# Kernel optimization log

Measured on AMD Instinct MI355X. Metric: run time of the kernel, lower is better.

## Reference

```python
import jax, jax.numpy as jnp
import numpy as np

GAMMA = 0.1      # rbf kernel gamma (args.sigma)
REG = 0.1        # diagonal regularizer (args.reg)
C = 1.0          # box constraint (args.C)
ETA = 0.001      # PGD step size (args.eta)
NUM_ITER = 100   # max solver iterations (args.num_iter)
STOP = 0.01      # relative-change stopping condition (args.stop_condition)
BS, D = 384, 256


def setup_inputs() -> dict:
    key = jax.random.key(0)
    k1, k2, k3 = jax.random.split(key, 3)
    return {
        "xis": jax.random.normal(k1, (BS, D), jnp.float32),
        "xjs": jax.random.normal(k2, (BS, D), jnp.float32),
        "alpha_init": jax.random.normal(k3, (BS, BS - 1, 1), jnp.float32),
    }


def _l2norm(x):
    return x / jnp.linalg.norm(x, axis=1, keepdims=True)


def _offdiag_idx(bs):
    # idx[i] = [0..bs-1] with i removed, shape (bs, bs-1); static, built with numpy
    idx = np.stack([np.concatenate([np.arange(i), np.arange(i + 1, bs)]) for i in range(bs)])
    return jnp.asarray(idx, dtype=jnp.int32)


def _pgd_nesterov(DD, lbd, alpha0):
    # min_a 0.5 a^T DD a - lbd^T a  s.t. 0 <= a <= C, batched over anchors,
    # Nesterov momentum beta_t = t/(t+3), early stop on relative change.
    def cond(state):
        t, a, a_prev, rel = state
        return (t < NUM_ITER) & (rel >= STOP)

    def body(state):
        t, a, a_prev, rel = state
        beta = t.astype(jnp.float32) / (t.astype(jnp.float32) + 3.0)
        z = a + beta * (a - a_prev)
        grad = jnp.einsum('bij,bjk->bik', DD, z) - lbd  # (bs, bs-1, 1)
        a_new = jnp.clip(jax.nn.relu(z - ETA * grad), 0.0, C)
        rel = jnp.linalg.norm(a_new - a) / (jnp.linalg.norm(a) + 1e-8)
        return (t + 1, a_new, a, rel)

    state = (jnp.array(0, jnp.int32), alpha0, alpha0, jnp.array(jnp.inf, jnp.float32))
    _, a, _, _ = jax.lax.while_loop(cond, body, state)
    return a


def _forward(xis, xjs, alpha_init):
    zis = _l2norm(xis)
    zjs = _l2norm(xjs)
    bs = zis.shape[0]
    Z = jnp.concatenate([zis, zjs], axis=0)          # (2bs, d)
    # rbf kernel: exp(-gamma * ||x - y||^2)
    sq = (jnp.sum(zis * zis, 1)[:, None] + jnp.sum(Z * Z, 1)[None, :]
          - 2.0 * zis @ Z.T)
    K = jnp.exp(-GAMMA * jnp.maximum(sq, 0.0))        # (bs, 2bs)

    KK = K[:, :bs]                                    # k(zis_i, zis_j)
    KK_d0 = KK * (1.0 - jnp.eye(bs, dtype=K.dtype))   # zero diagonal
    oneone = jnp.ones((bs, bs), K.dtype) + REG * jnp.eye(bs, dtype=K.dtype)
    # Delta[i,j,k] = 1 + reg*d_jk + KK[j,k] - KK_d0[i,j] - KK_d0[i,k]
    Delta = (oneone + KK)[None, :, :] - KK_d0[:, :, None] - KK_d0[:, None, :]

    idx = _offdiag_idx(bs)                            # (bs, bs-1)
    DD = jnp.take_along_axis(Delta, idx[:, :, None], axis=1)
    DD = jnp.take_along_axis(DD, idx[:, None, :], axis=2)  # (bs, bs-1, bs-1)

    alpha0 = jnp.clip(jax.nn.relu(alpha_init), 0.0, C)
    lbd = 2.0 * jnp.ones((bs, bs - 1, 1), K.dtype)
    alpha_y = _pgd_nesterov(jax.lax.stop_gradient(DD), lbd,
                            jax.lax.stop_gradient(alpha0))
    alpha_y = jax.lax.stop_gradient(jnp.clip(jax.nn.relu(alpha_y[:, :, 0]), 0.0, C))
    alpha_x = alpha_y.sum(1)                          # (bs,)

    Ks = K[:, bs:]                                    # k(zis_i, zjs_j), (bs, bs)
    pos_loss = jnp.mean(alpha_x * jnp.diagonal(Ks))
    # Kn[k,i] = Ks[idx[i,k], i]  -> gather off-diagonal of Ks.T per row
    KsT_offdiag = jnp.take_along_axis(Ks.T, idx, axis=1)  # (bs, bs-1)
    neg_loss = jnp.sum(alpha_y * KsT_offdiag) / bs
    return jnp.exp(neg_loss - pos_loss)


def reference(xis, xjs, alpha_init):
    return _forward(xis, xjs, alpha_init)
```

## Files before the change

### kernel.cpp

```cpp
#include <hip/hip_runtime.h>
#include <hip/hip_fp16.h>
#include <math.h>

#define BSZ   384
#define BM1   383
#define DIM   256
#define NZTOT 768
#define NBLK  96
#define RPB   4
#define TPB   768
#define NITER 100
#define RINGD 8
#define ARRFULL NBLK
#define KLDSU (16 * 5 * 384)
#define KRESB (KLDSU * 4)
#define WSHB  (4 * 384 * 4)
#define DYNB  (KRESB + WSHB)

#define OFF_Z    0
#define OFF_NRM  196608
#define OFF_K    197376
#define OFF_KH   492288
#define OFF_A    639744
#define OFF_NUM  786816
#define OFF_DEN  786944
#define OFF_ARR  787072
#define OFF_LOSS 787200

typedef _Float16 half8_t __attribute__((ext_vector_type(8)));
typedef float    f32x4_t __attribute__((ext_vector_type(4)));
__device__ __forceinline__ half8_t u4h8(uint4 v) {
    union { uint4 u; half8_t h; } x; x.u = v; return x.h;
}

__global__ void init_kernel(float* num, float* den, int* arr, double* lossAcc) {
    int t = threadIdx.x;
    if (t < NITER) { num[t] = 0.f; den[t] = 0.f; arr[t] = 0; }
    if (t < 2) lossAcc[t] = 0.0;
}

__global__ void __launch_bounds__(64)
norm_kernel(const float* __restrict__ xis, const float* __restrict__ xjs,
            float* __restrict__ Z, float* __restrict__ nrm2) {
    const int row  = blockIdx.x;
    const int lane = threadIdx.x;
    const float* src = (row < BSZ) ? (xis + (size_t)row * DIM)
                                   : (xjs + (size_t)(row - BSZ) * DIM);
    float4 x = reinterpret_cast<const float4*>(src)[lane];
    float s = x.x*x.x + x.y*x.y + x.z*x.z + x.w*x.w;
    for (int m = 32; m; m >>= 1) s += __shfl_xor(s, m, 64);
    float nrm = sqrtf(s);
    float4 z;
    z.x = x.x / nrm; z.y = x.y / nrm; z.z = x.z / nrm; z.w = x.w / nrm;
    reinterpret_cast<float4*>(Z + (size_t)row * DIM)[lane] = z;
    float s2 = z.x*z.x + z.y*z.y + z.z*z.z + z.w*z.w;
    for (int m = 32; m; m >>= 1) s2 += __shfl_xor(s2, m, 64);
    if (lane == 0) nrm2[row] = s2;
}

__global__ void __launch_bounds__(256)
k_kernel(const float* __restrict__ Z, const float* __restrict__ nrm2,
         float* __restrict__ Km, __half* __restrict__ KP2) {
    const int i = blockIdx.x;
    const int j = blockIdx.y * 256 + threadIdx.x;
    __shared__ float zi[DIM];
    zi[threadIdx.x] = Z[(size_t)i * DIM + threadIdx.x];
    __syncthreads();
    const float4* zr = reinterpret_cast<const float4*>(Z + (size_t)j * DIM);
    float acc = 0.f;
    #pragma unroll 8
    for (int k = 0; k < DIM/4; ++k) {
        float4 v = zr[k];
        acc = fmaf(zi[4*k+0], v.x, acc);
        acc = fmaf(zi[4*k+1], v.y, acc);
        acc = fmaf(zi[4*k+2], v.z, acc);
        acc = fmaf(zi[4*k+3], v.w, acc);
    }
    float sq = nrm2[i] + nrm2[j] - 2.f * acc;
    sq = fmaxf(sq, 0.f);
    const float val = expf(-0.1f * sq);
    Km[(size_t)i * NZTOT + j] = val;
    if (j < BSZ) KP2[(size_t)(i >> 1) * 768 + j * 2 + (i & 1)] = __float2half(val);
}

#define LDSFRAG(dst, s, t) do {                                               \
    const unsigned* _b = kresu + (16*(s) + kgrp*4)*384 + (c0 + 16*(t) + mloc);\
    dst.x = _b[0]; dst.y = _b[384]; dst.z = _b[768]; dst.w = _b[1152];        \
} while (0)

#define GFRAG(dst, s, t) do {                                                 \
    const unsigned* _b = kp2u + (size_t)(16*(s) + kgrp*4)*384 + (c0 + 16*(t) + mloc); \
    dst.x = _b[0]; dst.y = _b[384]; dst.z = _b[768]; dst.w = _b[1152];        \
} while (0)

#define BFRAG(dst, s) do {                                                    \
    dst = *reinterpret_cast<const uint4*>(&zh[rB][16*(s) + kgrp*4]);          \
} while (0)

#define STEP_LDS(s) do { uint4 _bf, _a0, _a1;                                 \
    BFRAG(_bf, s); LDSFRAG(_a0, s, 0); LDSFRAG(_a1, s, 1);                    \
    acc0 = __builtin_amdgcn_mfma_f32_16x16x32_f16(u4h8(_a0), u4h8(_bf), acc0, 0, 0, 0); \
    acc1 = __builtin_amdgcn_mfma_f32_16x16x32_f16(u4h8(_a1), u4h8(_bf), acc1, 0, 0, 0); \
} while (0)

#define STEP_REG(s, QA, QB) do { uint4 _bf;                                   \
    BFRAG(_bf, s);                                                            \
    acc0 = __builtin_amdgcn_mfma_f32_16x16x32_f16(u4h8(QA), u4h8(_bf), acc0, 0, 0, 0); \
    acc1 = __builtin_amdgcn_mfma_f32_16x16x32_f16(u4h8(QB), u4h8(_bf), acc1, 0, 0, 0); \
} while (0)

__global__ void __launch_bounds__(TPB, 1)
pgd_kernel(const float* __restrict__ Km, const __half* __restrict__ KP2,
           const float* __restrict__ alpha_init,
           float* __restrict__ afin, float* num, float* den, int* arr) {
    const int g    = blockIdx.x;
    const int c    = threadIdx.x;
    const int lane = c & 63;
    const int wv   = c >> 6;
    const int mloc = lane & 15;
    const int kgrp = lane >> 4;
    const int c0   = 32 * wv;
    const int rB   = mloc & 3;

    extern __shared__ char dynlc[];
    unsigned* const kresu = (unsigned*)dynlc;
    float* const    wshf  = (float*)(dynlc + KRESB);

    __shared__ unsigned zh[RPB][200];
    __shared__ float  rscr[12][10];
    __shared__ float  SD[8];
    __shared__ unsigned long long scanm[2];

    const bool act = (c < BSZ);
    const unsigned* const kp2u = (const unsigned*)KP2;

    float a[RPB], kb[RPB]; bool vld[RPB];
    #pragma unroll
    for (int r = 0; r < RPB; ++r) {
        const int b = g * RPB + r;
        vld[r] = act && (c != b);
        kb[r]  = act ? Km[(size_t)b * NZTOT + c] : 0.f;
        float v = 0.f;
        if (vld[r]) {
            const int i = c - (c > b ? 1 : 0);
            v = alpha_init[(size_t)b * BM1 + i];
            v = fminf(fmaxf(v, 0.f), 1.f);
        }
        a[r] = v;
    }
    float z[RPB];
    #pragma unroll
    for (int r = 0; r < RPB; ++r) z[r] = a[r];

    unsigned histx[RINGD], histy[RINGD];
    {
        const __half2 h01 = __floats2half2_rn(a[0], a[1]);
        const __half2 h23 = __floats2half2_rn(a[2], a[3]);
        const unsigned px = *reinterpret_cast<const unsigned*>(&h01);
        const unsigned py = *reinterpret_cast<const unsigned*>(&h23);
        #pragma unroll
        for (int s = 0; s < RINGD; ++s) { histx[s] = px; histy[s] = py; }
    }

    {
        const uint4* s4 = reinterpret_cast<const uint4*>(KP2);
        uint4* d4 = reinterpret_cast<uint4*>(kresu);
        #pragma unroll
        for (int i = 0; i < 10; ++i) d4[c + 768 * i] = s4[c + 768 * i];
    }
    uint4 q50,q51, q60,q61, q70,q71, q80,q81;
    GFRAG(q50, 5, 0); GFRAG(q51, 5, 1);
    GFRAG(q60, 6, 0); GFRAG(q61, 6, 1);
    GFRAG(q70, 7, 0); GFRAG(q71, 7, 1);
    GFRAG(q80, 8, 0); GFRAG(q81, 8, 1);

    {
        float an2 = 0.f;
        float vv[10];
        #pragma unroll
        for (int r = 0; r < RPB; ++r) {
            if (act) reinterpret_cast<__half*>(&zh[r][0])[c] = __float2half(z[r]);
            vv[r]     = z[r];
            vv[4 + r] = kb[r] * z[r];
            an2 += a[r] * a[r];
        }
        vv[8] = 0.f; vv[9] = an2;
        #pragma unroll
        for (int k = 0; k < 10; ++k) {
            float x = vv[k];
            x += __shfl_down(x, 32, 64); x += __shfl_down(x, 16, 64);
            x += __shfl_down(x,  8, 64); x += __shfl_down(x,  4, 64);
            x += __shfl_down(x,  2, 64); x += __shfl_down(x,  1, 64);
            if (lane == 0) rscr[wv][k] = x;
        }
        if (c < 2) scanm[c] = 0ULL;
    }
    __syncthreads();

    int stopT = -1;
    int sstate = 0, okv = 0, aval = 0;
    float nnv = 0.f, ddv = 1.f;

    for (int t = 0; t < NITER; ++t) {
        {
            const unsigned long long m0 = scanm[0], m1 = scanm[1];
            const int st = m0 ? (__ffsll(m0) - 1) : (m1 ? 63 + __ffsll(m1) : -1);
            if (st >= 0) { stopT = st; break; }
        }
        if (c < 8) {
            float s = 0.f;
            #pragma unroll
            for (int w = 0; w < 12; ++w) s += rscr[w][c];
            SD[c] = s;
        }
        if (c == 0) {
            float nb = 0.f, db = 0.f;
            #pragma unroll
            for (int w = 0; w < 12; ++w) { nb += rscr[w][8]; db += rscr[w][9]; }
            __hip_atomic_fetch_add(&den[t], db, __ATOMIC_RELAXED, __HIP_MEMORY_SCOPE_AGENT);
            if (t > 0) {
                __hip_atomic_fetch_add(&num[t - 1], nb, __ATOMIC_RELAXED, __HIP_MEMORY_SCOPE_AGENT);
                __hip_atomic_fetch_add(&arr[t - 1], 1, __ATOMIC_RELEASE, __HIP_MEMORY_SCOPE_AGENT);
            }
        }
        if (c < NITER) {
            if (sstate == 0) {
                aval = __hip_atomic_load(&arr[c], __ATOMIC_RELAXED, __HIP_MEMORY_SCOPE_AGENT);
            } else if (sstate == 1) {
                nnv = __hip_atomic_load(&num[c], __ATOMIC_RELAXED, __HIP_MEMORY_SCOPE_AGENT);
                ddv = __hip_atomic_load(&den[c], __ATOMIC_RELAXED, __HIP_MEMORY_SCOPE_AGENT);
            }
        }

        f32x4_t acc0 = {0.f, 0.f, 0.f, 0.f};
        f32x4_t acc1 = {0.f, 0.f, 0.f, 0.f};
        {
            uint4 g90,g91, gA0,gA1, gB0,gB1;
            GFRAG(g90,  9, 0); GFRAG(g91,  9, 1);
            GFRAG(gA0, 10, 0); GFRAG(gA1, 10, 1);
            GFRAG(gB0, 11, 0); GFRAG(gB1, 11, 1);
            STEP_LDS(0); STEP_LDS(1); STEP_LDS(2); STEP_LDS(3); STEP_LDS(4);
            STEP_REG(5, q50, q51);
            STEP_REG(6, q60, q61);
            STEP_REG(7, q70, q71);
            STEP_REG(8, q80, q81);
            STEP_REG(9,  g90, g91);
            STEP_REG(10, gA0, gA1);
            STEP_REG(11, gB0, gB1);
        }
        if (mloc < 4) {
            *reinterpret_cast<f32x4_t*>(&wshf[mloc * 384 + c0 + kgrp * 4])      = acc0;
            *reinterpret_cast<f32x4_t*>(&wshf[mloc * 384 + c0 + 16 + kgrp * 4]) = acc1;
        }
        __syncthreads();

        float nump = 0.f, an2 = 0.f;
        float zn[RPB] = {0.f, 0.f, 0.f, 0.f};
        float anA[RPB] = {0.f, 0.f, 0.f, 0.f};
        if (act) {
            const float beta1 = (float)(t + 1) / ((float)(t + 1) + 3.0f);
            #pragma unroll
            for (int r = 0; r < RPB; ++r) {
                const float w = wshf[r * 384 + c];
                float an = 0.f;
                if (vld[r]) {
                    const float grad = SD[r] * (1.f - kb[r]) + 0.1f * z[r] + w - SD[4 + r] - 2.0f;
                    an = z[r] - 0.001f * grad;
                    an = fminf(fmaxf(an, 0.f), 1.f);
                }
                const float d = an - a[r];
                nump += d * d;
                an2  += an * an;
                zn[r] = an + beta1 * (an - a[r]);
                anA[r] = an;
                a[r] = an;
            }
            #pragma unroll
            for (int r = 0; r < RPB; ++r) {
                reinterpret_cast<__half*>(&zh[r][0])[c] = __float2half(zn[r]);
                z[r] = zn[r];
            }
        }
        {
            const int slot = t & (RINGD - 1);
            const __half2 h01 = __floats2half2_rn(anA[0], anA[1]);
            const __half2 h23 = __floats2half2_rn(anA[2], anA[3]);
            const unsigned px = *reinterpret_cast<const unsigned*>(&h01);
            const unsigned py = *reinterpret_cast<const unsigned*>(&h23);
            #pragma unroll
            for (int s2 = 0; s2 < RINGD; ++s2) {
                histx[s2] = (s2 == slot) ? px : histx[s2];
                histy[s2] = (s2 == slot) ? py : histy[s2];
            }
        }
        {
            float vv[10] = { zn[0], zn[1], zn[2], zn[3],
                             kb[0]*zn[0], kb[1]*zn[1], kb[2]*zn[2], kb[3]*zn[3],
                             nump, an2 };
            #pragma unroll
            for (int k = 0; k < 10; ++k) {
                float x = vv[k];
                x += __shfl_down(x, 32, 64); x += __shfl_down(x, 16, 64);
                x += __shfl_down(x,  8, 64); x += __shfl_down(x,  4, 64);
                x += __shfl_down(x,  2, 64); x += __shfl_down(x,  1, 64);
                if (lane == 0) rscr[wv][k] = x;
            }
        }
        if (c < NITER) {
            if (sstate == 0) { if (aval == ARRFULL) sstate = 1; }
            else if (sstate == 1) {
                okv = (sqrtf(nnv) / (sqrtf(ddv) + 1e-8f) < 0.01f) ? 1 : 0;
                sstate = 2;
            }
        }
        {
            const unsigned long long bm = __ballot(okv);
            if (lane == 0 && wv < 2) scanm[wv] = bm;
        }
        __syncthreads();
    }

    float av[RPB];
    #pragma unroll
    for (int r = 0; r < RPB; ++r) av[r] = a[r];
    if (stopT >= 0) {
        unsigned sx = histx[0], sy = histy[0];
        const int sl = stopT & (RINGD - 1);
        #pragma unroll
        for (int s2 = 0; s2 < RINGD; ++s2) {
            sx = (s2 == sl) ? histx[s2] : sx;
            sy = (s2 == sl) ? histy[s2] : sy;
        }
        const float2 f01 = __half22float2(*reinterpret_cast<const __half2*>(&sx));
        const float2 f23 = __half22float2(*reinterpret_cast<const __half2*>(&sy));
        av[0] = f01.x; av[1] = f01.y; av[2] = f23.x; av[3] = f23.y;
    }
    if (act) {
        #pragma unroll
        for (int r = 0; r < RPB; ++r) {
            const int b = g * RPB + r;
            if (vld[r]) {
                const int i = c - (c > b ? 1 : 0);
                afin[(size_t)b * BM1 + i] = av[r];
            }
        }
    }
}

__global__ void __launch_bounds__(384)
loss_kernel(const float* __restrict__ Km, const float* __restrict__ afin,
            double* lossAcc) {
    const int b    = blockIdx.x;
    const int tid  = threadIdx.x;
    const int lane = tid & 63;
    const int wv   = tid >> 6;
    __shared__ double dscr[6][2];
    double np = 0.0, pp = 0.0;
    if (tid < BM1) {
        const float ay = afin[(size_t)b * BM1 + tid];
        const int   I  = tid + (tid >= b);
        np = (double)ay * (double)Km[(size_t)I * NZTOT + BSZ + b];
        pp = (double)ay * (double)Km[(size_t)b * NZTOT + BSZ + b];
    }
    for (int o = 32; o; o >>= 1) { np += __shfl_down(np, o, 64); pp += __shfl_down(pp, o, 64); }
    if (lane == 0) { dscr[wv][0] = np; dscr[wv][1] = pp; }
    __syncthreads();
    if (tid == 0) {
        double nb = 0.0, pb = 0.0;
        for (int w = 0; w < 6; ++w) { nb += dscr[w][0]; pb += dscr[w][1]; }
        __hip_atomic_fetch_add(&lossAcc[0], nb, __ATOMIC_RELAXED, __HIP_MEMORY_SCOPE_AGENT);
        __hip_atomic_fetch_add(&lossAcc[1], pb, __ATOMIC_RELAXED, __HIP_MEMORY_SCOPE_AGENT);
    }
}

__global__ void fin_kernel(const double* lossAcc, float* out) {
    out[0] = expf((float)(lossAcc[0] / 384.0 - lossAcc[1] / 384.0));
}

extern "C" void kernel_launch(void* const* d_in, const int* in_sizes, int n_in,
                              void* d_out, int out_size, void* d_ws, size_t ws_size,
                              hipStream_t stream) {
    const float* xis        = (const float*)d_in[0];
    const float* xjs        = (const float*)d_in[1];
    const float* alpha_init = (const float*)d_in[2];
    float* ws   = (float*)d_ws;
    float* Z    = ws + OFF_Z;
    float* nrm2 = ws + OFF_NRM;
    float* Km   = ws + OFF_K;
    __half* KP2 = (__half*)(ws + OFF_KH);
    float* afin = ws + OFF_A;
    float* num  = ws + OFF_NUM;
    float* den  = ws + OFF_DEN;
    int*   arr  = (int*)(ws + OFF_ARR);
    double* lossAcc = (double*)(ws + OFF_LOSS);
    float* out  = (float*)d_out;

    hipFuncSetAttribute((const void*)pgd_kernel,
                        hipFuncAttributeMaxDynamicSharedMemorySize, DYNB);

    hipLaunchKernelGGL(init_kernel, dim3(1), dim3(128), 0, stream, num, den, arr, lossAcc);
    hipLaunchKernelGGL(norm_kernel, dim3(NZTOT), dim3(64), 0, stream, xis, xjs, Z, nrm2);
    hipLaunchKernelGGL(k_kernel, dim3(BSZ, 3), dim3(256), 0, stream, Z, nrm2, Km, KP2);
    hipLaunchKernelGGL(pgd_kernel, dim3(NBLK), dim3(TPB), DYNB, stream,
                       Km, KP2, alpha_init, afin, num, den, arr);
    hipLaunchKernelGGL(loss_kernel, dim3(BSZ), dim3(384), 0, stream, Km, afin, lossAcc);
    hipLaunchKernelGGL(fin_kernel, dim3(1), dim3(1), 0, stream, lossAcc, out);
}
```

Baseline: 649.1 us.

## Pad LDS K pitch and prepack global K fragments into MFMA-ready uint4 layout

Stores the LDS-resident part of the K matrix with a padded row pitch of 388 words so the strided fragment reads avoid bank conflicts. A new pack kernel rewrites the global K fragments into a contiguous uint4-per-lane layout, so the per-iteration global fragment fetches become single 16-byte loads instead of four strided 4-byte loads. The cost is an extra kernel launch, a scratch buffer that reuses the Z workspace region, and a slower scalar LDS fill loop with division.

```diff
diff --git a/kernel.cpp b/kernel.cpp
--- a/kernel.cpp
+++ b/kernel.cpp
@@ -12,11 +12,12 @@
 #define NITER 100
 #define RINGD 8
 #define ARRFULL NBLK
-#define KLDSU (16 * 5 * 384)
-#define KRESB (KLDSU * 4)
+#define PITCH 388
+#define KRESB (80 * PITCH * 4)
 #define WSHB  (4 * 384 * 4)
 #define DYNB  (KRESB + WSHB)
 
+#define OFF_KF   0
 #define OFF_Z    0
 #define OFF_NRM  196608
 #define OFF_K    197376
@@ -83,14 +84,30 @@
     if (j < BSZ) KP2[(size_t)(i >> 1) * 768 + j * 2 + (i & 1)] = __float2half(val);
 }
 
+__global__ void __launch_bounds__(256)
+pack_kernel(const __half* __restrict__ KP2, unsigned* __restrict__ KF) {
+    const int idx = blockIdx.x * 256 + threadIdx.x;
+    if (idx >= 12 * 384 * 4) return;
+    const unsigned* src = (const unsigned*)KP2;
+    const int kgrp = idx & 3;
+    const int col  = (idx >> 2) % 384;
+    const int s    = idx / (384 * 4);
+    const int row0 = 16 * s + kgrp * 4;
+    uint4 v;
+    v.x = src[(row0 + 0) * 384 + col];
+    v.y = src[(row0 + 1) * 384 + col];
+    v.z = src[(row0 + 2) * 384 + col];
+    v.w = src[(row0 + 3) * 384 + col];
+    reinterpret_cast<uint4*>(KF)[idx] = v;
+}
+
 #define LDSFRAG(dst, s, t) do {                                               \
-    const unsigned* _b = kresu + (16*(s) + kgrp*4)*384 + (c0 + 16*(t) + mloc);\
-    dst.x = _b[0]; dst.y = _b[384]; dst.z = _b[768]; dst.w = _b[1152];        \
+    const unsigned* _b = kresu + (16*(s) + kgrp*4)*PITCH + (c0 + 16*(t) + mloc); \
+    dst.x = _b[0]; dst.y = _b[PITCH]; dst.z = _b[2*PITCH]; dst.w = _b[3*PITCH]; \
 } while (0)
 
-#define GFRAG(dst, s, t) do {                                                 \
-    const unsigned* _b = kp2u + (size_t)(16*(s) + kgrp*4)*384 + (c0 + 16*(t) + mloc); \
-    dst.x = _b[0]; dst.y = _b[384]; dst.z = _b[768]; dst.w = _b[1152];        \
+#define KFFRAG(dst, s, t) do {                                                \
+    dst = kfu4[((s)*384 + (c0 + 16*(t) + mloc))*4 + kgrp];                    \
 } while (0)
 
 #define BFRAG(dst, s) do {                                                    \
@@ -111,6 +128,7 @@
 
 __global__ void __launch_bounds__(TPB, 1)
 pgd_kernel(const float* __restrict__ Km, const __half* __restrict__ KP2,
+           const unsigned* __restrict__ KF,
            const float* __restrict__ alpha_init,
            float* __restrict__ afin, float* num, float* den, int* arr) {
     const int g    = blockIdx.x;
@@ -133,6 +151,7 @@
 
     const bool act = (c < BSZ);
     const unsigned* const kp2u = (const unsigned*)KP2;
+    const uint4* const kfu4 = (const uint4*)KF;
 
     float a[RPB], kb[RPB]; bool vld[RPB];
     #pragma unroll
@@ -162,17 +181,17 @@
         for (int s = 0; s < RINGD; ++s) { histx[s] = px; histy[s] = py; }
     }
 
-    {
-        const uint4* s4 = reinterpret_cast<const uint4*>(KP2);
-        uint4* d4 = reinterpret_cast<uint4*>(kresu);
-        #pragma unroll
-        for (int i = 0; i < 10; ++i) d4[c + 768 * i] = s4[c + 768 * i];
+    for (int i = 0; i < 40; ++i) {
+        const int j   = c + 768 * i;
+        const int row = j / 384;
+        const int col = j - row * 384;
+        kresu[row * PITCH + col] = kp2u[j];
     }
     uint4 q50,q51, q60,q61, q70,q71, q80,q81;
-    GFRAG(q50, 5, 0); GFRAG(q51, 5, 1);
-    GFRAG(q60, 6, 0); GFRAG(q61, 6, 1);
-    GFRAG(q70, 7, 0); GFRAG(q71, 7, 1);
-    GFRAG(q80, 8, 0); GFRAG(q81, 8, 1);
+    KFFRAG(q50, 5, 0); KFFRAG(q51, 5, 1);
+    KFFRAG(q60, 6, 0); KFFRAG(q61, 6, 1);
+    KFFRAG(q70, 7, 0); KFFRAG(q71, 7, 1);
+    KFFRAG(q80, 8, 0); KFFRAG(q81, 8, 1);
 
     {
         float an2 = 0.f;
@@ -236,9 +255,9 @@
         f32x4_t acc1 = {0.f, 0.f, 0.f, 0.f};
         {
             uint4 g90,g91, gA0,gA1, gB0,gB1;
-            GFRAG(g90,  9, 0); GFRAG(g91,  9, 1);
-            GFRAG(gA0, 10, 0); GFRAG(gA1, 10, 1);
-            GFRAG(gB0, 11, 0); GFRAG(gB1, 11, 1);
+            KFFRAG(g90,  9, 0); KFFRAG(g91,  9, 1);
+            KFFRAG(gA0, 10, 0); KFFRAG(gA1, 10, 1);
+            KFFRAG(gB0, 11, 0); KFFRAG(gB1, 11, 1);
             STEP_LDS(0); STEP_LDS(1); STEP_LDS(2); STEP_LDS(3); STEP_LDS(4);
             STEP_REG(5, q50, q51);
             STEP_REG(6, q60, q61);
@@ -385,6 +404,7 @@
     const float* alpha_init = (const float*)d_in[2];
     float* ws   = (float*)d_ws;
     float* Z    = ws + OFF_Z;
+    unsigned* KF = (unsigned*)(ws + OFF_KF);
     float* nrm2 = ws + OFF_NRM;
     float* Km   = ws + OFF_K;
     __half* KP2 = (__half*)(ws + OFF_KH);
@@ -401,8 +421,9 @@
     hipLaunchKernelGGL(init_kernel, dim3(1), dim3(128), 0, stream, num, den, arr, lossAcc);
     hipLaunchKernelGGL(norm_kernel, dim3(NZTOT), dim3(64), 0, stream, xis, xjs, Z, nrm2);
     hipLaunchKernelGGL(k_kernel, dim3(BSZ, 3), dim3(256), 0, stream, Z, nrm2, Km, KP2);
+    hipLaunchKernelGGL(pack_kernel, dim3(72), dim3(256), 0, stream, KP2, KF);
     hipLaunchKernelGGL(pgd_kernel, dim3(NBLK), dim3(TPB), DYNB, stream,
-                       Km, KP2, alpha_init, afin, num, den, arr);
+                       Km, KP2, KF, alpha_init, afin, num, den, arr);
     hipLaunchKernelGGL(loss_kernel, dim3(BSZ), dim3(384), 0, stream, Km, afin, lossAcc);
     hipLaunchKernelGGL(fin_kernel, dim3(1), dim3(1), 0, stream, lossAcc, out);
 }
```

Result: no change. 655.4 us (+1.0%).
